# Optimization experiments

Measured on AMD Instinct MI355X. Metric: run time of the kernel, lower is better.

Reference implementation:

```python
import jax, jax.numpy as jnp
import numpy as np

B, T, S, D = 8, 2048, 8, 256


def setup_inputs() -> dict:
    key = jax.random.key(0)
    k1, k2, k3 = jax.random.split(key, 3)
    x = jax.random.normal(k1, (B, T, S, D), dtype=jnp.float32)
    # nn.Linear-style init scale ~ 1/sqrt(fan_in)
    W_in = jax.random.normal(k2, (D, 2 * D), dtype=jnp.float32) / np.sqrt(D)
    b_in = jnp.zeros((2 * D,), dtype=jnp.float32)
    W_out = jax.random.normal(k3, (D, D), dtype=jnp.float32) / np.sqrt(D)
    b_out = jnp.zeros((D,), dtype=jnp.float32)
    return {"x": x, "W_in": W_in, "b_in": b_in, "W_out": W_out, "b_out": b_out}


def reference(x, W_in, b_in, W_out, b_out):
    # in_proj then chunk into gate / candidate (matches torch chunk(2, dim=-1))
    h = jnp.einsum("btsd,de->btse", x, W_in) + b_in  # [B,T,S,2D]
    gate, cand = jnp.split(h, 2, axis=-1)
    alpha = jax.nn.sigmoid(gate)
    cand = jnp.tanh(cand)
    # Diagonal linear recurrence: state_t = a_t * state_{t-1} + b_t
    # with a_t = 1 - alpha_t, b_t = alpha_t * cand_t, state_{-1} = 0.
    a = 1.0 - alpha
    b = alpha * cand

    def combine(c1, c2):
        a1, b1 = c1
        a2, b2 = c2
        return a1 * a2, a2 * b1 + b2

    _, y = jax.lax.associative_scan(combine, (a, b), axis=1)  # [B,T,S,D]
    # dropout is identity in eval mode
    return jnp.einsum("btsd,de->btse", y, W_out) + b_out
```

## Files before the change

kernel.cpp:

```cpp
#include <hip/hip_runtime.h>
#include <hip/hip_bf16.h>
#include <hip/hip_fp16.h>
#include <cstdint>

typedef __attribute__((ext_vector_type(4))) float f32x4;
typedef __attribute__((ext_vector_type(8))) short s16x8;

#define DEVI static __device__ __forceinline__

constexpr int Bc = 8, Tc = 2048, Sc = 8, Dc = 256;
constexpr int Mc = Bc * Tc * Sc;

DEVI unsigned short f2bf(float x) {
  return __bfloat16_as_ushort(__float2bfloat16(x));
}

DEVI f32x4 mfma16(s16x8 a, s16x8 b, f32x4 c) {
  return __builtin_amdgcn_mfma_f32_16x16x32_bf16(a, b, c, 0, 0, 0);
}

DEVI void gld16(const void* g, void* l) {
  __builtin_amdgcn_global_load_lds(
      (const __attribute__((address_space(1))) unsigned int*)g,
      (__attribute__((address_space(3))) unsigned int*)l, 16, 0, 0);
}

__global__ void cvt_x_k(const float* __restrict__ in, unsigned short* __restrict__ out, int n) {
  int i = (blockIdx.x * blockDim.x + threadIdx.x) * 8;
  int stride = gridDim.x * blockDim.x * 8;
  for (; i < n; i += stride) {
    f32x4 a = *(const f32x4*)(in + i);
    f32x4 b = *(const f32x4*)(in + i + 4);
    s16x8 o;
    o[0] = (short)f2bf(a[0]); o[1] = (short)f2bf(a[1]);
    o[2] = (short)f2bf(a[2]); o[3] = (short)f2bf(a[3]);
    o[4] = (short)f2bf(b[0]); o[5] = (short)f2bf(b[1]);
    o[6] = (short)f2bf(b[2]); o[7] = (short)f2bf(b[3]);
    *(s16x8*)(out + i) = o;
  }
}

__global__ void cvtW_k(const float* __restrict__ Win, const float* __restrict__ Wout,
                       unsigned short* __restrict__ wtin, unsigned short* __restrict__ wtout) {
  int tid = blockIdx.x * blockDim.x + threadIdx.x;
  if (tid < 512 * 256) {
    int c = tid >> 8, r = tid & 255;
    wtin[tid] = f2bf(Win[r * 512 + c]);
  } else {
    int t = tid - 512 * 256;
    int c = t >> 8, r = t & 255;
    wtout[t] = f2bf(Wout[r * 256 + c]);
  }
}

__global__ __launch_bounds__(512, 2) void g1scan_k(
    const unsigned short* __restrict__ xb,
    const unsigned short* __restrict__ wt,
    const float* __restrict__ bias,
    unsigned short* __restrict__ yb)
{
  __shared__ unsigned short As[2][8 * 64 * 32];
  __shared__ float segA[2][4][32], segB[2][4][32];

  int bid = blockIdx.x;
  int lb = (bid & 7) * 64 + (bid >> 3);
  int b = lb >> 6, s = (lb >> 3) & 7, dq = lb & 7;
  int tid = threadIdx.x;
  int lane = tid & 63, wave = tid >> 6;
  int rg = wave >> 1, cg = wave & 1;
  int lo = lane & 15, hi = lane >> 4;

  const short* xs = (const short*)xb;
  const short* wsrc = (const short*)wt;
  size_t rowbase = (size_t)b * 16384 + s;

  int cl = cg * 16 + lo;
  int kg = hi * 8;

  s16x8 bGr[8], bCr[8];
  #pragma unroll
  for (int kf = 0; kf < 8; ++kf) {
    bGr[kf] = *(const s16x8*)(wsrc + (size_t)(dq * 32 + cl) * 256 + kf * 32 + kg);
    bCr[kf] = *(const s16x8*)(wsrc + (size_t)(256 + dq * 32 + cl) * 256 + kf * 32 + kg);
  }
  float bg = bias[dq * 32 + cl];
  float bc = bias[256 + dq * 32 + cl];

  const short* pA[4];
  int ldso[4];
  #pragma unroll
  for (int q = 0; q < 4; ++q) {
    int j = q * 512 + tid;
    int kf = j >> 8, rem = j & 255, r = rem >> 2, cc = j & 3;
    pA[q] = xs + (rowbase + (size_t)r * 8) * 256 + kf * 32 + cc * 8;
    ldso[q] = j * 8;
  }
  const size_t ASTRIDE = (size_t)64 * 8 * 256;

  #pragma unroll
  for (int q = 0; q < 4; ++q) gld16(pA[q], (unsigned short*)As[0] + ldso[q]);
  #pragma unroll
  for (int q = 0; q < 4; ++q) gld16(pA[q] + ASTRIDE, (unsigned short*)As[1] + ldso[q]);
  #pragma unroll
  for (int q = 0; q < 4; ++q) pA[q] += 2 * ASTRIDE;

  float stt = 0.f;

  __syncthreads();

  for (int ch = 0; ch < 32; ++ch) {
    int cur = ch & 1;
    const unsigned short* Ab = (const unsigned short*)As[cur];

    f32x4 accG = {}, accC = {};
    #pragma unroll
    for (int kf = 0; kf < 8; ++kf) {
      s16x8 aF = *(const s16x8*)(Ab + kf * 2048 + (rg * 16 + lo) * 32 + kg);
      accG = mfma16(aF, bGr[kf], accG);
      accC = mfma16(aF, bCr[kf], accC);
    }

    float av[4], bv[4];
    #pragma unroll
    for (int r = 0; r < 4; ++r) {
      float g = accG[r] + bg;
      float c = accC[r] + bc;
      float eg = __expf(-g);
      float alpha = __builtin_amdgcn_rcpf(1.f + eg);
      float e2 = __expf(2.f * c);
      float th = 1.f - 2.f * __builtin_amdgcn_rcpf(e2 + 1.f);
      av[r] = 1.f - alpha;
      bv[r] = alpha * th;
    }

    float iA = av[0], iB = bv[0];
    #pragma unroll
    for (int r = 1; r < 4; ++r) { iA = iA * av[r]; iB = fmaf(av[r], iB, bv[r]); }

    {
      float tA = __shfl_up(iA, 16), tB = __shfl_up(iB, 16);
      float nA = tA * iA, nB = fmaf(iA, tB, iB);
      if (hi >= 1) { iA = nA; iB = nB; }
      tA = __shfl_up(iA, 32); tB = __shfl_up(iB, 32);
      nA = tA * iA; nB = fmaf(iA, tB, iB);
      if (hi >= 2) { iA = nA; iB = nB; }
    }
    float eA = __shfl_up(iA, 16), eB = __shfl_up(iB, 16);
    if (hi == 0) { eA = 1.f; eB = 0.f; }
    if (hi == 3) { segA[cur][rg][cl] = iA; segB[cur][rg][cl] = iB; }

    __syncthreads();

    if (ch + 2 < 32) {
      #pragma unroll
      for (int q = 0; q < 4; ++q) gld16(pA[q], (unsigned short*)As[cur] + ldso[q]);
      #pragma unroll
      for (int q = 0; q < 4; ++q) pA[q] += ASTRIDE;
    }

    float run = stt, s_w = stt;
    #pragma unroll
    for (int r2 = 0; r2 < 4; ++r2) {
      if (r2 == rg) s_w = run;
      run = fmaf(segA[cur][r2][cl], run, segB[cur][r2][cl]);
    }
    stt = run;

    float sv = fmaf(eA, s_w, eB);
    size_t ybase = (rowbase + (size_t)(ch * 64 + rg * 16 + hi * 4) * 8) * 256 + dq * 32 + cl;
    #pragma unroll
    for (int u = 0; u < 4; ++u) {
      sv = fmaf(av[u], sv, bv[u]);
      yb[ybase + (size_t)u * 8 * 256] = f2bf(sv);
    }
  }
}

__global__ __launch_bounds__(256, 2) void gemm2_k(
    const unsigned short* __restrict__ yb,
    const unsigned short* __restrict__ wt,
    const float* __restrict__ bias,
    float* __restrict__ out)
{
  __shared__ unsigned short As[2][2][128 * 32];
  __shared__ unsigned short Bs[2][2][128 * 32];

  int bid = blockIdx.x;
  int swz = (bid & 7) * 256 + (bid >> 3);
  int mtile = swz >> 1, ctile = swz & 1;
  int tid = threadIdx.x;
  int lane = tid & 63, wave = tid >> 6;
  int wr = wave >> 1, wc = wave & 1;

  const short* ys = (const short*)yb;
  const short* wsrc = (const short*)wt;

  auto STAGE = [&](int buf, int k0) {
    unsigned short* Ad = &As[buf][0][0];
    unsigned short* Bd = &Bs[buf][0][0];
    #pragma unroll
    for (int q = 0; q < 4; ++q) {
      int j = q * 256 + tid;
      int p = j >> 9, r = (j >> 2) & 127, cc = j & 3;
      int koff = k0 + p * 32 + cc * 8;
      gld16(ys + (size_t)(mtile * 128 + r) * 256 + koff, Ad + (size_t)j * 8);
      gld16(wsrc + (size_t)(ctile * 128 + r) * 256 + koff, Bd + (size_t)j * 8);
    }
  };

  f32x4 acc[4][4] = {};

  STAGE(0, 0);
  __syncthreads();
  #pragma unroll
  for (int kk = 0; kk < 4; ++kk) {
    int cur = kk & 1;
    if (kk < 3) STAGE(cur ^ 1, (kk + 1) * 64);
    int kg = (lane >> 4) * 8;
    #pragma unroll
    for (int ks = 0; ks < 2; ++ks) {
      s16x8 aF[4], bF[4];
      #pragma unroll
      for (int mf = 0; mf < 4; ++mf)
        aF[mf] = *(const s16x8*)&As[cur][ks][(wr * 64 + mf * 16 + (lane & 15)) * 32 + kg];
      #pragma unroll
      for (int nf = 0; nf < 4; ++nf)
        bF[nf] = *(const s16x8*)&Bs[cur][ks][(wc * 64 + nf * 16 + (lane & 15)) * 32 + kg];
      #pragma unroll
      for (int mf = 0; mf < 4; ++mf)
        #pragma unroll
        for (int nf = 0; nf < 4; ++nf)
          acc[mf][nf] = mfma16(aF[mf], bF[nf], acc[mf][nf]);
    }
    if (kk < 3) __syncthreads();
  }

  int orow0 = mtile * 128 + wr * 64 + (lane >> 4) * 4;
  #pragma unroll
  for (int nf = 0; nf < 4; ++nf) {
    int col = ctile * 128 + wc * 64 + nf * 16 + (lane & 15);
    float bo = bias[col];
    #pragma unroll
    for (int mf = 0; mf < 4; ++mf) {
      #pragma unroll
      for (int r = 0; r < 4; ++r) {
        int row = orow0 + mf * 16 + r;
        out[(size_t)row * 256 + col] = acc[mf][nf][r] + bo;
      }
    }
  }
}

extern "C" void kernel_launch(void* const* d_in, const int* in_sizes, int n_in,
                              void* d_out, int out_size, void* d_ws, size_t ws_size,
                              hipStream_t stream)
{
  const float* x    = (const float*)d_in[0];
  const float* Win  = (const float*)d_in[1];
  const float* bin  = (const float*)d_in[2];
  const float* Wout = (const float*)d_in[3];
  const float* bout = (const float*)d_in[4];
  float* out = (float*)d_out;
  char* ws = (char*)d_ws;

  unsigned short* wtin  = (unsigned short*)(ws);
  unsigned short* wtout = (unsigned short*)(ws + 262144);
  unsigned short* yb    = (unsigned short*)(ws + 393216);
  unsigned short* xb    = (unsigned short*)(ws + 393216 + (size_t)Mc * 256 * 2);

  cvt_x_k<<<1024, 256, 0, stream>>>(x, xb, Mc * 256);
  cvtW_k<<<768, 256, 0, stream>>>(Win, Wout, wtin, wtout);
  g1scan_k<<<512, 512, 0, stream>>>(xb, wtin, bin, yb);
  gemm2_k<<<2048, 256, 0, stream>>>(yb, wtout, bout, out);
}
```

Before: 155.3 us.

## Fuse fp32-to-bf16 conversion of x into the projection-scan kernel

Drops the separate x conversion kernel. The scan kernel now loads fp32 x straight into registers, converts it to bf16 and writes it to LDS, with a one-chunk-ahead register prefetch. This replaces the async global-to-LDS loads and removes the extra bf16 copy of x that was written to and read back from global memory. Launch bounds are raised to 4 blocks per CU, which tightens the register budget and risks spills, since the kernel now also holds the prefetch registers.

```diff
diff --git a/kernel.cpp b/kernel.cpp
--- a/kernel.cpp
+++ b/kernel.cpp
@@ -15,6 +15,15 @@
   return __bfloat16_as_ushort(__float2bfloat16(x));
 }
 
+DEVI s16x8 cvt8(f32x4 a, f32x4 b) {
+  s16x8 o;
+  o[0] = (short)f2bf(a[0]); o[1] = (short)f2bf(a[1]);
+  o[2] = (short)f2bf(a[2]); o[3] = (short)f2bf(a[3]);
+  o[4] = (short)f2bf(b[0]); o[5] = (short)f2bf(b[1]);
+  o[6] = (short)f2bf(b[2]); o[7] = (short)f2bf(b[3]);
+  return o;
+}
+
 DEVI f32x4 mfma16(s16x8 a, s16x8 b, f32x4 c) {
   return __builtin_amdgcn_mfma_f32_16x16x32_bf16(a, b, c, 0, 0, 0);
 }
@@ -23,21 +32,6 @@
   __builtin_amdgcn_global_load_lds(
       (const __attribute__((address_space(1))) unsigned int*)g,
       (__attribute__((address_space(3))) unsigned int*)l, 16, 0, 0);
-}
-
-__global__ void cvt_x_k(const float* __restrict__ in, unsigned short* __restrict__ out, int n) {
-  int i = (blockIdx.x * blockDim.x + threadIdx.x) * 8;
-  int stride = gridDim.x * blockDim.x * 8;
-  for (; i < n; i += stride) {
-    f32x4 a = *(const f32x4*)(in + i);
-    f32x4 b = *(const f32x4*)(in + i + 4);
-    s16x8 o;
-    o[0] = (short)f2bf(a[0]); o[1] = (short)f2bf(a[1]);
-    o[2] = (short)f2bf(a[2]); o[3] = (short)f2bf(a[3]);
-    o[4] = (short)f2bf(b[0]); o[5] = (short)f2bf(b[1]);
-    o[6] = (short)f2bf(b[2]); o[7] = (short)f2bf(b[3]);
-    *(s16x8*)(out + i) = o;
-  }
 }
 
 __global__ void cvtW_k(const float* __restrict__ Win, const float* __restrict__ Wout,
@@ -53,8 +47,8 @@
   }
 }
 
-__global__ __launch_bounds__(512, 2) void g1scan_k(
-    const unsigned short* __restrict__ xb,
+__global__ __launch_bounds__(512, 4) void g1scan_k(
+    const float* __restrict__ x,
     const unsigned short* __restrict__ wt,
     const float* __restrict__ bias,
     unsigned short* __restrict__ yb)
@@ -70,7 +64,6 @@
   int rg = wave >> 1, cg = wave & 1;
   int lo = lane & 15, hi = lane >> 4;
 
-  const short* xs = (const short*)xb;
   const short* wsrc = (const short*)wt;
   size_t rowbase = (size_t)b * 16384 + s;
 
@@ -86,26 +79,36 @@
   float bg = bias[dq * 32 + cl];
   float bc = bias[256 + dq * 32 + cl];
 
-  const short* pA[4];
+  const float* pF[4];
   int ldso[4];
   #pragma unroll
   for (int q = 0; q < 4; ++q) {
     int j = q * 512 + tid;
     int kf = j >> 8, rem = j & 255, r = rem >> 2, cc = j & 3;
-    pA[q] = xs + (rowbase + (size_t)r * 8) * 256 + kf * 32 + cc * 8;
+    pF[q] = x + (rowbase + (size_t)r * 8) * 256 + kf * 32 + cc * 8;
     ldso[q] = j * 8;
   }
   const size_t ASTRIDE = (size_t)64 * 8 * 256;
 
-  #pragma unroll
-  for (int q = 0; q < 4; ++q) gld16(pA[q], (unsigned short*)As[0] + ldso[q]);
-  #pragma unroll
-  for (int q = 0; q < 4; ++q) gld16(pA[q] + ASTRIDE, (unsigned short*)As[1] + ldso[q]);
-  #pragma unroll
-  for (int q = 0; q < 4; ++q) pA[q] += 2 * ASTRIDE;
-
+  f32x4 pa[4][2];
+  auto LDF = [&]() {
+    #pragma unroll
+    for (int q = 0; q < 4; ++q) {
+      pa[q][0] = *(const f32x4*)(pF[q]);
+      pa[q][1] = *(const f32x4*)(pF[q] + 4);
+      pF[q] += ASTRIDE;
+    }
+  };
+  auto WRF = [&](int buf) {
+    #pragma unroll
+    for (int q = 0; q < 4; ++q)
+      *(s16x8*)((unsigned short*)As[buf] + ldso[q]) = cvt8(pa[q][0], pa[q][1]);
+  };
+
+  LDF();
+  WRF(0);
+  LDF();
   float stt = 0.f;
-
   __syncthreads();
 
   for (int ch = 0; ch < 32; ++ch) {
@@ -149,14 +152,11 @@
     if (hi == 0) { eA = 1.f; eB = 0.f; }
     if (hi == 3) { segA[cur][rg][cl] = iA; segB[cur][rg][cl] = iB; }
 
+    if (ch + 1 < 32) WRF(cur ^ 1);
+
     __syncthreads();
 
-    if (ch + 2 < 32) {
-      #pragma unroll
-      for (int q = 0; q < 4; ++q) gld16(pA[q], (unsigned short*)As[cur] + ldso[q]);
-      #pragma unroll
-      for (int q = 0; q < 4; ++q) pA[q] += ASTRIDE;
-    }
+    if (ch + 2 < 32) LDF();
 
     float run = stt, s_w = stt;
     #pragma unroll
@@ -266,10 +266,8 @@
   unsigned short* wtin  = (unsigned short*)(ws);
   unsigned short* wtout = (unsigned short*)(ws + 262144);
   unsigned short* yb    = (unsigned short*)(ws + 393216);
-  unsigned short* xb    = (unsigned short*)(ws + 393216 + (size_t)Mc * 256 * 2);
-
-  cvt_x_k<<<1024, 256, 0, stream>>>(x, xb, Mc * 256);
+
   cvtW_k<<<768, 256, 0, stream>>>(Win, Wout, wtin, wtout);
-  g1scan_k<<<512, 512, 0, stream>>>(xb, wtin, bin, yb);
+  g1scan_k<<<512, 512, 0, stream>>>(x, wtin, bin, yb);
   gemm2_k<<<2048, 256, 0, stream>>>(yb, wtout, bout, out);
 }
```

Result: slower. 203.2 us (+30.8%).
